# Optimization experiments

Measured on AMD Instinct MI355X. Metric: run time of the kernel, lower is better.

The kernel has to match this reference:

```python
import jax, jax.numpy as jnp
import numpy as np

B, E, H, NH, HD = 8, 1536, 256, 8, 32
L, V, NL, FF = 50, 50257, 4, 2048
BOS = 50256
EPS = 1e-5


def setup_inputs():
    key = jax.random.key(0)
    ks = jax.random.split(key, 12)
    s = 0.02

    def rn(k, shape):
        return jax.random.normal(k, shape, jnp.float32) * s

    return {
        "embedding": jax.random.normal(ks[0], (B, E), jnp.float32),
        "w_proj": rn(ks[1], (H, E)), "b_proj": jnp.zeros((H,), jnp.float32),
        "tok_emb": rn(ks[2], (V, H)),
        "pos_enc": rn(ks[3], (1, L, H)),
        "sa_in_w": rn(ks[4], (NL, 3 * H, H)), "sa_in_b": jnp.zeros((NL, 3 * H), jnp.float32),
        "sa_out_w": rn(ks[5], (NL, H, H)), "sa_out_b": jnp.zeros((NL, H), jnp.float32),
        "ca_in_w": rn(ks[6], (NL, 3 * H, H)), "ca_in_b": jnp.zeros((NL, 3 * H), jnp.float32),
        "ca_out_w": rn(ks[7], (NL, H, H)), "ca_out_b": jnp.zeros((NL, H), jnp.float32),
        "ff1_w": rn(ks[8], (NL, FF, H)), "ff1_b": jnp.zeros((NL, FF), jnp.float32),
        "ff2_w": rn(ks[9], (NL, H, FF)), "ff2_b": jnp.zeros((NL, H), jnp.float32),
        "ln_g": jnp.ones((NL, 3, H), jnp.float32), "ln_b": jnp.zeros((NL, 3, H), jnp.float32),
        "fc_w": rn(ks[10], (V, H)), "fc_b": jnp.zeros((V,), jnp.float32),
    }


def _ln(x, g, b):
    m = jnp.mean(x, -1, keepdims=True)
    v = jnp.mean((x - m) ** 2, -1, keepdims=True)
    return (x - m) * jax.lax.rsqrt(v + EPS) * g + b


def _mha(q_in, kv_in, in_w, in_b, out_w, out_b, mask):
    wq, wk, wv = jnp.split(in_w, 3, axis=0)
    bq, bk, bv = jnp.split(in_b, 3)

    def heads(t):
        b_, l_, _ = t.shape
        return t.reshape(b_, l_, NH, HD).transpose(0, 2, 1, 3)  # [B,NH,L,HD]

    q = heads(q_in @ wq.T + bq)
    k = heads(kv_in @ wk.T + bk)
    v = heads(kv_in @ wv.T + bv)
    scores = jnp.einsum('bhqd,bhkd->bhqk', q, k) * (1.0 / np.sqrt(HD))
    if mask is not None:
        scores = scores + mask
    a = jax.nn.softmax(scores, axis=-1)
    o = jnp.einsum('bhqk,bhkd->bhqd', a, v)
    o = o.transpose(0, 2, 1, 3).reshape(q_in.shape)
    return o @ out_w.T + out_b


def _decoder(x, mem, mask, p):
    # nn.TransformerDecoderLayer, post-LN, relu FFN
    for l in range(NL):
        x = _ln(x + _mha(x, x, p['sa_in_w'][l], p['sa_in_b'][l], p['sa_out_w'][l], p['sa_out_b'][l], mask), p['ln_g'][l, 0], p['ln_b'][l, 0])
        x = _ln(x + _mha(x, mem, p['ca_in_w'][l], p['ca_in_b'][l], p['ca_out_w'][l], p['ca_out_b'][l], None), p['ln_g'][l, 1], p['ln_b'][l, 1])
        h = jax.nn.relu(x @ p['ff1_w'][l].T + p['ff1_b'][l]) @ p['ff2_w'][l].T + p['ff2_b'][l]
        x = _ln(x + h, p['ln_g'][l, 2], p['ln_b'][l, 2])
    return x


def _forward(embedding, tok_emb, pos_enc, w_proj, b_proj, fc_w, fc_b, p):
    mem = (embedding @ w_proj.T + b_proj)[:, None, :]  # [B,1,H] single-token memory
    causal = jnp.tril(jnp.ones((L, L), bool))
    mask = jnp.where(causal, 0.0, -jnp.inf)[None, None]  # [1,1,L,L]
    tokens0 = jnp.full((B, L), BOS, jnp.int32)  # padded token buffer; pos 0 = BOS

    # At step t the original recomputes the decoder over the first t+1 tokens and
    # reads the last position. With a causal mask, position t of a full-length
    # decode depends only on tokens[:t+1], so decoding the padded buffer and
    # slicing position t is exactly the same math (no-KV-cache recompute kept).
    def step(tokens, t):
        x = tok_emb[tokens] + pos_enc[:, :L]
        x = _decoder(x, mem, mask, p)
        h_t = jax.lax.dynamic_slice_in_dim(x, t, 1, axis=1)[:, 0]  # [B,H]
        logits = h_t @ fc_w.T + fc_b  # [B,V]
        nxt = jnp.argmax(logits, -1).astype(jnp.int32)
        tokens = jax.lax.dynamic_update_slice_in_dim(tokens, nxt[:, None], t + 1, axis=1)
        return tokens, logits

    _, logits = jax.lax.scan(step, tokens0, jnp.arange(L - 1))
    return jnp.transpose(logits, (1, 0, 2))  # [B, L-1, V]


def reference(embedding, w_proj, b_proj, tok_emb, pos_enc, sa_in_w, sa_in_b, sa_out_w, sa_out_b, ca_in_w, ca_in_b, ca_out_w, ca_out_b, ff1_w, ff1_b, ff2_w, ff2_b, ln_g, ln_b, fc_w, fc_b):
    p = dict(sa_in_w=sa_in_w, sa_in_b=sa_in_b, sa_out_w=sa_out_w, sa_out_b=sa_out_b,
             ca_in_w=ca_in_w, ca_in_b=ca_in_b, ca_out_w=ca_out_w, ca_out_b=ca_out_b,
             ff1_w=ff1_w, ff1_b=ff1_b, ff2_w=ff2_w, ff2_b=ff2_b, ln_g=ln_g, ln_b=ln_b)
    return _forward(embedding, tok_emb, pos_enc, w_proj, b_proj, fc_w, fc_b, p)
```

## Files before the change

### kernel.cpp

```cpp
#include <hip/hip_runtime.h>

#define NV 50257
#define BOSTOK 50256
#define LNEPS 1e-5f
#define NSTEP 49
#define NBLK 256
#define RPB 197
#define DYN_LDS_BYTES ((256 * 52 + 50 * 256) * 4)
#define FSTR 64

#define FQKV(l)   (0 + (l))
#define FU(l)     (4 + (l))
#define FFPX(l,j) (8 + (l) * 8 + (j))
#define FXF(j)    (40 + (j))
#define FFC(j)    (48 + (j))
#define FMEMF     56
#define FCAF      57

#define WS4_MEM 4096
#define WS4_CA  6144
#define WS4_XF  14336
#define WS4_Q   16384
#define WS4_K   18432
#define WS4_V   20480
#define WS4_U   22528
#define WS4_FFP 30720
#define WS4_PV  63488
#define WS4_PI  65536

__device__ __forceinline__ float gld(const float* p) {
  return __hip_atomic_load(const_cast<float*>(p), __ATOMIC_RELAXED, __HIP_MEMORY_SCOPE_AGENT);
}
__device__ __forceinline__ void gst(float* p, float v) {
  __hip_atomic_store(p, v, __ATOMIC_RELAXED, __HIP_MEMORY_SCOPE_AGENT);
}
__device__ __forceinline__ void gsti(int* p, int v) {
  __hip_atomic_store(p, v, __ATOMIC_RELAXED, __HIP_MEMORY_SCOPE_AGENT);
}
__device__ __forceinline__ unsigned fld(unsigned* p) {
  return __hip_atomic_load(p, __ATOMIC_RELAXED, __HIP_MEMORY_SCOPE_AGENT);
}
__device__ __forceinline__ void bump(unsigned* f) {
  asm volatile("s_waitcnt vmcnt(0)" ::: "memory");
  __syncthreads();
  if (threadIdx.x == 0)
    __hip_atomic_fetch_add(f, 1u, __ATOMIC_RELAXED, __HIP_MEMORY_SCOPE_AGENT);
}
__device__ __forceinline__ void bump8(unsigned* f) {
  asm volatile("s_waitcnt vmcnt(0)" ::: "memory");
  __syncthreads();
  if (threadIdx.x == 0)
    for (int j = 0; j < 8; ++j)
      __hip_atomic_fetch_add(f + j * FSTR, 1u, __ATOMIC_RELAXED, __HIP_MEMORY_SCOPE_AGENT);
}
__device__ __forceinline__ unsigned waitf(unsigned* f, unsigned tgt, unsigned* sh) {
  if (threadIdx.x == 0) {
    unsigned v = fld(f);
    while (v < tgt) { __builtin_amdgcn_s_sleep(1); v = fld(f); }
    *sh = v;
  }
  __syncthreads();
  return *sh;
}
__device__ __forceinline__ unsigned wait_fcsum(unsigned* FL, unsigned tgt, unsigned* sh) {
  if (threadIdx.x == 0) {
    unsigned s;
    for (;;) {
      s = 0;
      for (int j = 0; j < 8; ++j) s += fld(FL + (48 + j) * FSTR);
      if (s >= tgt) break;
      __builtin_amdgcn_s_sleep(1);
    }
    *sh = s;
  }
  __syncthreads();
  return *sh;
}

__device__ __forceinline__ void pull2p(float* x, float* y,
    const float* p0, const float* p1, unsigned salt) {
  asm("global_load_dword %0, %2, off sc0 sc1\n\t"
      "global_load_dword %1, %3, off sc0 sc1\n\t"
      "s_waitcnt vmcnt(0)"
      : "=&v"(*x), "=&v"(*y)
      : "v"(p0), "v"(p1), "v"(salt));
}
__device__ __forceinline__ void pull3p(float* x, float* y, float* z,
    const float* p0, const float* p1, const float* p2, unsigned salt) {
  asm("global_load_dword %0, %3, off sc0 sc1\n\t"
      "global_load_dword %1, %4, off sc0 sc1\n\t"
      "global_load_dword %2, %5, off sc0 sc1\n\t"
      "s_waitcnt vmcnt(0)"
      : "=&v"(*x), "=&v"(*y), "=&v"(*z)
      : "v"(p0), "v"(p1), "v"(p2), "v"(salt));
}
__device__ __forceinline__ void pull8p(float r[8],
    const float* p0, const float* p1, const float* p2, const float* p3,
    const float* p4, const float* p5, const float* p6, const float* p7, unsigned salt) {
  float a0, a1, a2, a3, a4, a5, a6, a7;
  asm("global_load_dword %0, %8, off sc0 sc1\n\t"
      "global_load_dword %1, %9, off sc0 sc1\n\t"
      "global_load_dword %2, %10, off sc0 sc1\n\t"
      "global_load_dword %3, %11, off sc0 sc1\n\t"
      "global_load_dword %4, %12, off sc0 sc1\n\t"
      "global_load_dword %5, %13, off sc0 sc1\n\t"
      "global_load_dword %6, %14, off sc0 sc1\n\t"
      "global_load_dword %7, %15, off sc0 sc1\n\t"
      "s_waitcnt vmcnt(0)"
      : "=&v"(a0), "=&v"(a1), "=&v"(a2), "=&v"(a3),
        "=&v"(a4), "=&v"(a5), "=&v"(a6), "=&v"(a7)
      : "v"(p0), "v"(p1), "v"(p2), "v"(p3), "v"(p4), "v"(p5), "v"(p6), "v"(p7), "v"(salt));
  r[0] = a0; r[1] = a1; r[2] = a2; r[3] = a3;
  r[4] = a4; r[5] = a5; r[6] = a6; r[7] = a7;
}
__device__ __forceinline__ void pull1_2q(float* u, float4* f0, float4* f1,
    const float* pu, const float* pf, unsigned salt) {
  asm("global_load_dword %0, %3, off sc0 sc1\n\t"
      "global_load_dwordx4 %1, %4, off sc0 sc1\n\t"
      "global_load_dwordx4 %2, %4, off offset:16 sc0 sc1\n\t"
      "s_waitcnt vmcnt(0)"
      : "=&v"(*u), "=&v"(*f0), "=&v"(*f1)
      : "v"(pu), "v"(pf), "v"(salt));
}
__device__ __forceinline__ void pull4x8(float4 r[8],
    const float* p0, const float* p1, const float* p2, const float* p3, unsigned salt) {
  float4 a0, a1, a2, a3, a4, a5, a6, a7;
  asm("global_load_dwordx4 %0, %8, off sc0 sc1\n\t"
      "global_load_dwordx4 %1, %8, off offset:16 sc0 sc1\n\t"
      "global_load_dwordx4 %2, %9, off sc0 sc1\n\t"
      "global_load_dwordx4 %3, %9, off offset:16 sc0 sc1\n\t"
      "global_load_dwordx4 %4, %10, off sc0 sc1\n\t"
      "global_load_dwordx4 %5, %10, off offset:16 sc0 sc1\n\t"
      "global_load_dwordx4 %6, %11, off sc0 sc1\n\t"
      "global_load_dwordx4 %7, %11, off offset:16 sc0 sc1\n\t"
      "s_waitcnt vmcnt(0)"
      : "=&v"(a0), "=&v"(a1), "=&v"(a2), "=&v"(a3),
        "=&v"(a4), "=&v"(a5), "=&v"(a6), "=&v"(a7)
      : "v"(p0), "v"(p1), "v"(p2), "v"(p3), "v"(salt));
  r[0] = a0; r[1] = a1; r[2] = a2; r[3] = a3;
  r[4] = a4; r[5] = a5; r[6] = a6; r[7] = a7;
}

__device__ __forceinline__ float block_ln256(float v, int tid, float* red8, float g, float bta) {
  float s = v, s2 = v * v;
#pragma unroll
  for (int m = 32; m >= 1; m >>= 1) { s += __shfl_xor(s, m); s2 += __shfl_xor(s2, m); }
  int w = tid >> 6;
  __syncthreads();
  if ((tid & 63) == 0) { red8[w] = s; red8[4 + w] = s2; }
  __syncthreads();
  s = red8[0] + red8[1] + red8[2] + red8[3];
  s2 = red8[4] + red8[5] + red8[6] + red8[7];
  float mn = s * (1.0f / 256.0f);
  float var = s2 * (1.0f / 256.0f) - mn * mn;
  float rs = rsqrtf(var + LNEPS);
  return (v - mn) * rs * g + bta;
}

__device__ __forceinline__ void fc_phase(int bid, int tid, int t, unsigned salt,
                                         const float* xf, const float* fc_w,
                                         const float* fc_b, float* out,
                                         float* pv, int* pi,
                                         float* xl, float* rv, int* ri) {
  {
    float xv8[8];
    pull8p(xv8, xf + 0 * 256 + tid, xf + 1 * 256 + tid, xf + 2 * 256 + tid, xf + 3 * 256 + tid,
           xf + 4 * 256 + tid, xf + 5 * 256 + tid, xf + 6 * 256 + tid, xf + 7 * 256 + tid, salt);
#pragma unroll
    for (int b = 0; b < 8; ++b) xl[b * 260 + tid] = xv8[b];
  }
  __syncthreads();
  int r = tid >> 3, b = tid & 7;
  float bv = -3e38f; int bi = 2147483647;
  int base = bid * RPB;
  for (int i = 0; i < 7; ++i) {
    int rr = i * 32 + r, row = base + rr;
    if (rr < RPB && row < NV) {
      float acc = fc_b[row];
      const float4* w4 = reinterpret_cast<const float4*>(fc_w + (size_t)row * 256);
      const float4* xv = reinterpret_cast<const float4*>(xl + b * 260);
      for (int k = 0; k < 64; ++k) {
        float4 wv = w4[k]; float4 xq = xv[k];
        acc += wv.x * xq.x + wv.y * xq.y + wv.z * xq.z + wv.w * xq.w;
      }
      out[(size_t)(b * 49 + t) * NV + row] = acc;
      if (acc > bv || (acc == bv && row < bi)) { bv = acc; bi = row; }
    }
  }
  rv[tid] = bv; ri[tid] = bi;
  __syncthreads();
  for (int off = 128; off >= 8; off >>= 1) {
    if (tid < off) {
      float v = rv[tid + off]; int id = ri[tid + off];
      if (v > rv[tid] || (v == rv[tid] && id < ri[tid])) { rv[tid] = v; ri[tid] = id; }
    }
    __syncthreads();
  }
  if (tid < 8) { gst(pv + bid * 8 + tid, rv[tid]); gsti(pi + bid * 8 + tid, ri[tid]); }
}

__global__ __launch_bounds__(256) void k_flow4(
    const float* __restrict__ emb, const float* __restrict__ w_proj, const float* __restrict__ b_proj,
    const float* __restrict__ tok_emb, const float* __restrict__ pos_enc,
    const float* __restrict__ sa_in_w, const float* __restrict__ sa_in_b,
    const float* __restrict__ sa_out_w, const float* __restrict__ sa_out_b,
    const float* __restrict__ ca_in_w, const float* __restrict__ ca_in_b,
    const float* __restrict__ ca_out_w, const float* __restrict__ ca_out_b,
    const float* __restrict__ ff1_w, const float* __restrict__ ff1_b,
    const float* __restrict__ ff2_w, const float* __restrict__ ff2_b,
    const float* __restrict__ ln_g, const float* __restrict__ ln_b,
    const float* __restrict__ fc_w, const float* __restrict__ fc_b,
    float* __restrict__ out, float* __restrict__ wsf, int* __restrict__ wsi) {
  extern __shared__ float dynlds[];
  const int bid = blockIdx.x, tid = threadIdx.x;

  unsigned* FL = (unsigned*)wsf;
  float* mem = wsf + WS4_MEM;
  float* ca  = wsf + WS4_CA;
  float* xf  = wsf + WS4_XF;
  float* qb  = wsf + WS4_Q;
  float* kb  = wsf + WS4_K;
  float* vb  = wsf + WS4_V;
  float* u   = wsf + WS4_U;
  float* ffp = wsf + WS4_FFP;
  float* pv  = wsf + WS4_PV;
  int*   pi  = wsi + WS4_PI;

  __shared__ float xl[8 * 260];
  __shared__ float h1l[256 * 9];
  __shared__ float ql[256], ol[256], ph[8 * 64];
  __shared__ float red8[8];
  __shared__ float rv[256];
  __shared__ int   ri[256];
  __shared__ int   toks[8];
  __shared__ unsigned saltsh;
  __shared__ float el[1536];

  if (bid < 64) {
    int b = bid >> 3, tile = bid & 7;
    for (int k = tid; k < 1536; k += 256) el[k] = emb[b * 1536 + k];
    __syncthreads();
    int r = tid >> 3, g = tid & 7;
    int row = tile * 32 + r;
    float acc = 0.f;
    const float* wr = w_proj + (size_t)row * 1536;
    for (int c = g * 192; c < g * 192 + 192; ++c) acc += wr[c] * el[c];
    rv[tid] = acc;
    __syncthreads();
    for (int off = 4; off >= 1; off >>= 1) {
      if (g < off) rv[tid] += rv[tid + off];
      __syncthreads();
    }
    if (g == 0) gst(mem + b * 256 + row, rv[tid] + b_proj[row]);
    bump(FL + FMEMF * FSTR);
  }
  if (bid >= 64 && bid < 96) {
    unsigned s0 = waitf(FL + FMEMF * FSTR, 64u, &saltsh);
    int l = (bid - 64) >> 3, b = (bid - 64) & 7;
    ql[tid] = gld(mem + b * 256 + tid) + 0.f * (float)(s0 & 0);
    __syncthreads();
    float acc = ca_in_b[l * 768 + 512 + tid];
    const float* wr = ca_in_w + (size_t)(l * 768 + 512 + tid) * 256;
    for (int c = 0; c < 256; ++c) acc += wr[c] * ql[c];
    ol[tid] = acc;
    __syncthreads();
    float acc2 = ca_out_b[l * 256 + tid];
    const float* wr2 = ca_out_w + (size_t)(l * 256 + tid) * 256;
    for (int c = 0; c < 256; ++c) acc2 += wr2[c] * ol[c];
    gst(ca + (l * 8 + b) * 256 + tid, acc2);
    bump(FL + FCAF * FSTR);
  }

  if (bid < 32) {
    int myl = bid >> 3, myb = bid & 7;
    float* Klds = dynlds;
    float* Vlds = dynlds + 256 * 52;
    unsigned sc = waitf(FL + FCAF * FSTR, 32u, &saltsh);
    float caval = gld(ca + ((myl * 8 + myb) * 256 + (int)(sc & 0)) + tid);
    for (int t = 0; t < NSTEP; ++t) {
      float xres;
      if (myl == 0) {
        if (t > 0) {
          unsigned s = wait_fcsum(FL, 256u * (unsigned)t, &saltsh);
          float pvv, piv;
          pull2p(&pvv, &piv, pv + tid * 8 + myb, (const float*)(pi + tid * 8 + myb), s);
          rv[tid] = pvv; ri[tid] = __float_as_int(piv);
          __syncthreads();
          for (int off = 128; off >= 1; off >>= 1) {
            if (tid < off) {
              float v = rv[tid + off]; int id = ri[tid + off];
              if (v > rv[tid] || (v == rv[tid] && id < ri[tid])) { rv[tid] = v; ri[tid] = id; }
            }
            __syncthreads();
          }
          if (tid == 0) toks[0] = ri[0];
          __syncthreads();
        } else {
          if (tid == 0) toks[0] = BOSTOK;
          __syncthreads();
        }
        xres = tok_emb[(size_t)toks[0] * 256 + tid] + pos_enc[t * 256 + tid];
      } else {
        unsigned s = waitf(FL + FFPX(myl - 1, bid & 7) * FSTR, 8u * (unsigned)(t + 1), &saltsh);
        float uv; float4 f0, f1;
        int par = (myl - 1) & 1;
        pull1_2q(&uv, &f0, &f1, u + (myl - 1) * 2048 + myb * 256 + tid,
                 ffp + par * 16384 + (myb * 256 + tid) * 8, s);
        float a = uv + ff2_b[(myl - 1) * 256 + tid]
                + f0.x + f0.y + f0.z + f0.w + f1.x + f1.y + f1.z + f1.w;
        xres = block_ln256(a, tid, red8, ln_g[((myl - 1) * 3 + 2) * 256 + tid],
                           ln_b[((myl - 1) * 3 + 2) * 256 + tid]);
      }
      unsigned s2 = waitf(FL + FQKV(myl) * FSTR, 24u * (unsigned)(t + 1), &saltsh);
      float qv, kv, vv;
      pull3p(&qv, &kv, &vv, qb + myb * 256 + tid, kb + myb * 256 + tid, vb + myb * 256 + tid, s2);
      ql[tid] = qv;
      Klds[tid * 52 + t] = kv;
      Vlds[t * 256 + tid] = vv;
      __syncthreads();
      int h = tid >> 5, j0 = tid & 31;
      const float* qh = ql + h * 32;
      float s0v = -3e38f, s1v = -3e38f;
      if (j0 <= t) {
        float d0 = 0.f;
#pragma unroll
        for (int d = 0; d < 32; ++d) d0 += qh[d] * Klds[(h * 32 + d) * 52 + j0];
        s0v = d0 * 0.17677669529663687f;
      }
      if (j0 + 32 <= t) {
        float d1 = 0.f;
#pragma unroll
        for (int d = 0; d < 32; ++d) d1 += qh[d] * Klds[(h * 32 + d) * 52 + j0 + 32];
        s1v = d1 * 0.17677669529663687f;
      }
      float mx = fmaxf(s0v, s1v);
      for (int m = 16; m >= 1; m >>= 1) mx = fmaxf(mx, __shfl_xor(mx, m, 32));
      float e0 = (j0 <= t) ? expf(s0v - mx) : 0.f;
      float e1 = (j0 + 32 <= t) ? expf(s1v - mx) : 0.f;
      float sm = e0 + e1;
      for (int m = 16; m >= 1; m >>= 1) sm += __shfl_xor(sm, m, 32);
      ph[h * 64 + j0] = e0;
      ph[h * 64 + j0 + 32] = e1;
      __syncthreads();
      float o = 0.f;
      for (int j = 0; j <= t; ++j) o += ph[h * 64 + j] * Vlds[j * 256 + tid];
      ol[tid] = o / sm;
      __syncthreads();
      float acc = sa_out_b[myl * 256 + tid];
      const float4* w4 = reinterpret_cast<const float4*>(sa_out_w + (size_t)(myl * 256 + tid) * 256);
#pragma unroll 4
      for (int k = 0; k < 64; ++k) {
        float4 wv = w4[k];
        acc += wv.x * ol[4 * k] + wv.y * ol[4 * k + 1] + wv.z * ol[4 * k + 2] + wv.w * ol[4 * k + 3];
      }
      acc += xres;
      float y = block_ln256(acc, tid, red8, ln_g[(myl * 3 + 0) * 256 + tid],
                            ln_b[(myl * 3 + 0) * 256 + tid]);
      float y2 = block_ln256(y + caval, tid, red8,
                             ln_g[(myl * 3 + 1) * 256 + tid], ln_b[(myl * 3 + 1) * 256 + tid]);
      gst(u + myl * 2048 + myb * 256 + tid, y2);
      bump(FL + FU(myl) * FSTR);

      if (myl == 0) {
        unsigned s3 = waitf(FL + FFPX(3, bid & 7) * FSTR, 8u * (unsigned)(t + 1), &saltsh);
        float uv; float4 f0, f1;
        pull1_2q(&uv, &f0, &f1, u + 3 * 2048 + myb * 256 + tid,
                 ffp + 1 * 16384 + (myb * 256 + tid) * 8, s3);
        float a = uv + ff2_b[3 * 256 + tid]
                + f0.x + f0.y + f0.z + f0.w + f1.x + f1.y + f1.z + f1.w;
        float xfv = block_ln256(a, tid, red8, ln_g[(3 * 3 + 2) * 256 + tid],
                                ln_b[(3 * 3 + 2) * 256 + tid]);
        gst(xf + myb * 256 + tid, xfv);
        bump8(FL + FXF(0) * FSTR);
      }
      unsigned s4 = waitf(FL + FXF(bid & 7) * FSTR, 8u * (unsigned)(t + 1), &saltsh);
      fc_phase(bid, tid, t, s4, xf, fc_w, fc_b, out, pv, pi, xl, rv, ri);
      bump(FL + FFC(bid & 7) * FSTR);
    }
  } else if (bid < 56) {
    int qi = bid - 32;
    for (int t = 0; t < NSTEP; ++t) {
      for (int l = 0; l < 4; ++l) {
        if (l == 0) {
          if (t == 0) {
            if (tid < 8) toks[tid] = BOSTOK;
            __syncthreads();
          } else {
            unsigned s = wait_fcsum(FL, 256u * (unsigned)t, &saltsh);
            int i0 = tid >> 3, b = tid & 7;
            float pvv[8], piv[8];
            pull8p(pvv, pv + (i0 + 0) * 8 + b, pv + (i0 + 32) * 8 + b, pv + (i0 + 64) * 8 + b,
                   pv + (i0 + 96) * 8 + b, pv + (i0 + 128) * 8 + b, pv + (i0 + 160) * 8 + b,
                   pv + (i0 + 192) * 8 + b, pv + (i0 + 224) * 8 + b, s);
            const float* pif = (const float*)pi;
            pull8p(piv, pif + (i0 + 0) * 8 + b, pif + (i0 + 32) * 8 + b, pif + (i0 + 64) * 8 + b,
                   pif + (i0 + 96) * 8 + b, pif + (i0 + 128) * 8 + b, pif + (i0 + 160) * 8 + b,
                   pif + (i0 + 192) * 8 + b, pif + (i0 + 224) * 8 + b, s);
            float bv = -3e38f; int bi = 2147483647;
#pragma unroll
            for (int k = 0; k < 8; ++k) {
              float v = pvv[k]; int id = __float_as_int(piv[k]);
              if (v > bv || (v == bv && id < bi)) { bv = v; bi = id; }
            }
            rv[tid] = bv; ri[tid] = bi;
            __syncthreads();
            for (int off = 128; off >= 8; off >>= 1) {
              if (tid < off) {
                float v = rv[tid + off]; int id = ri[tid + off];
                if (v > rv[tid] || (v == rv[tid] && id < ri[tid])) { rv[tid] = v; ri[tid] = id; }
              }
              __syncthreads();
            }
            if (tid < 8) toks[tid] = ri[tid];
            __syncthreads();
          }
          for (int b = 0; b < 8; ++b)
            xl[b * 260 + tid] = tok_emb[(size_t)toks[b] * 256 + tid] + pos_enc[t * 256 + tid];
          __syncthreads();
        } else {
          unsigned s = waitf(FL + FFPX(l - 1, bid & 7) * FSTR, 8u * (unsigned)(t + 1), &saltsh);
          int lp = l - 1, par = lp & 1;
          float u8[8];
          pull8p(u8, u + lp * 2048 + 0 * 256 + tid, u + lp * 2048 + 1 * 256 + tid,
                 u + lp * 2048 + 2 * 256 + tid, u + lp * 2048 + 3 * 256 + tid,
                 u + lp * 2048 + 4 * 256 + tid, u + lp * 2048 + 5 * 256 + tid,
                 u + lp * 2048 + 6 * 256 + tid, u + lp * 2048 + 7 * 256 + tid, s);
          float4 fA[8], fB[8];
          const float* fb = ffp + par * 16384;
          pull4x8(fA, fb + (0 * 256 + tid) * 8, fb + (1 * 256 + tid) * 8,
                  fb + (2 * 256 + tid) * 8, fb + (3 * 256 + tid) * 8, s);
          pull4x8(fB, fb + (4 * 256 + tid) * 8, fb + (5 * 256 + tid) * 8,
                  fb + (6 * 256 + tid) * 8, fb + (7 * 256 + tid) * 8, s);
          float g = ln_g[(lp * 3 + 2) * 256 + tid], bt = ln_b[(lp * 3 + 2) * 256 + tid];
          float f2b = ff2_b[lp * 256 + tid];
#pragma unroll
          for (int b = 0; b < 8; ++b) {
            float4 q0 = (b < 4) ? fA[2 * b] : fB[2 * (b - 4)];
            float4 q1 = (b < 4) ? fA[2 * b + 1] : fB[2 * (b - 4) + 1];
            float a = u8[b] + f2b + q0.x + q0.y + q0.z + q0.w + q1.x + q1.y + q1.z + q1.w;
            xl[b * 260 + tid] = block_ln256(a, tid, red8, g, bt);
          }
          __syncthreads();
        }
        int r = tid >> 3, b8 = tid & 7;
        int row = qi * 32 + r;
        float acc = sa_in_b[l * 768 + row];
        const float4* w4 = reinterpret_cast<const float4*>(sa_in_w + (size_t)(l * 768 + row) * 256);
        const float4* xv = reinterpret_cast<const float4*>(xl + b8 * 260);
#pragma unroll 8
        for (int k = 0; k < 64; ++k) {
          float4 wv = w4[k]; float4 xq = xv[k];
          acc += wv.x * xq.x + wv.y * xq.y + wv.z * xq.z + wv.w * xq.w;
        }
        if (row < 256) gst(qb + b8 * 256 + row, acc);
        else if (row < 512) gst(kb + b8 * 256 + (row - 256), acc);
        else gst(vb + b8 * 256 + (row - 512), acc);
        bump(FL + FQKV(l) * FSTR);
      }
      unsigned s4 = waitf(FL + FXF(bid & 7) * FSTR, 8u * (unsigned)(t + 1), &saltsh);
      fc_phase(bid, tid, t, s4, xf, fc_w, fc_b, out, pv, pi, xl, rv, ri);
      bump(FL + FFC(bid & 7) * FSTR);
    }
  } else if (bid < 64) {
    int s = bid - 56;
    for (int t = 0; t < NSTEP; ++t) {
      for (int l = 0; l < 4; ++l) {
        unsigned sv = waitf(FL + FU(l) * FSTR, 8u * (unsigned)(t + 1), &saltsh);
        {
          float u8[8];
          pull8p(u8, u + l * 2048 + 0 * 256 + tid, u + l * 2048 + 1 * 256 + tid,
                 u + l * 2048 + 2 * 256 + tid, u + l * 2048 + 3 * 256 + tid,
                 u + l * 2048 + 4 * 256 + tid, u + l * 2048 + 5 * 256 + tid,
                 u + l * 2048 + 6 * 256 + tid, u + l * 2048 + 7 * 256 + tid, sv);
#pragma unroll
          for (int b = 0; b < 8; ++b) xl[b * 260 + tid] = u8[b];
        }
        __syncthreads();
        {
          int row = s * 256 + tid;
          float acc[8];
          float bb = ff1_b[l * 2048 + row];
#pragma unroll
          for (int b = 0; b < 8; ++b) acc[b] = bb;
          const float4* w4 = reinterpret_cast<const float4*>(ff1_w + (size_t)(l * 2048 + row) * 256);
          for (int k = 0; k < 64; ++k) {
            float4 wv = w4[k];
#pragma unroll
            for (int b = 0; b < 8; ++b) {
              const float4 xq = reinterpret_cast<const float4*>(xl + b * 260)[k];
              acc[b] += wv.x * xq.x + wv.y * xq.y + wv.z * xq.z + wv.w * xq.w;
            }
          }
#pragma unroll
          for (int b = 0; b < 8; ++b) h1l[tid * 9 + b] = fmaxf(acc[b], 0.f);
        }
        __syncthreads();
        {
          float facc[8] = {0, 0, 0, 0, 0, 0, 0, 0};
          const float* w2p = ff2_w + (size_t)(l * 256 + tid) * 2048 + s * 256;
          for (int n = 0; n < 256; ++n) {
            float wv = w2p[n];
#pragma unroll
            for (int b = 0; b < 8; ++b) facc[b] += wv * h1l[n * 9 + b];
          }
          int par = l & 1;
#pragma unroll
          for (int b = 0; b < 8; ++b)
            gst(ffp + par * 16384 + (b * 256 + tid) * 8 + s, facc[b]);
        }
        bump8(FL + FFPX(l, 0) * FSTR);
        __syncthreads();
      }
      unsigned s4 = waitf(FL + FXF(bid & 7) * FSTR, 8u * (unsigned)(t + 1), &saltsh);
      fc_phase(bid, tid, t, s4, xf, fc_w, fc_b, out, pv, pi, xl, rv, ri);
      bump(FL + FFC(bid & 7) * FSTR);
    }
  } else {
    for (int t = 0; t < NSTEP; ++t) {
      unsigned s4 = waitf(FL + FXF(bid & 7) * FSTR, 8u * (unsigned)(t + 1), &saltsh);
      fc_phase(bid, tid, t, s4, xf, fc_w, fc_b, out, pv, pi, xl, rv, ri);
      bump(FL + FFC(bid & 7) * FSTR);
    }
  }
}

extern "C" void kernel_launch(void* const* d_in, const int* in_sizes, int n_in,
                              void* d_out, int out_size, void* d_ws, size_t ws_size,
                              hipStream_t stream) {
  (void)in_sizes; (void)n_in; (void)out_size; (void)ws_size;
  const float* embedding = (const float*)d_in[0];
  const float* w_proj   = (const float*)d_in[1];
  const float* b_proj   = (const float*)d_in[2];
  const float* tok_emb  = (const float*)d_in[3];
  const float* pos_enc  = (const float*)d_in[4];
  const float* sa_in_w  = (const float*)d_in[5];
  const float* sa_in_b  = (const float*)d_in[6];
  const float* sa_out_w = (const float*)d_in[7];
  const float* sa_out_b = (const float*)d_in[8];
  const float* ca_in_w  = (const float*)d_in[9];
  const float* ca_in_b  = (const float*)d_in[10];
  const float* ca_out_w = (const float*)d_in[11];
  const float* ca_out_b = (const float*)d_in[12];
  const float* ff1_w    = (const float*)d_in[13];
  const float* ff1_b    = (const float*)d_in[14];
  const float* ff2_w    = (const float*)d_in[15];
  const float* ff2_b    = (const float*)d_in[16];
  const float* ln_g     = (const float*)d_in[17];
  const float* ln_b     = (const float*)d_in[18];
  const float* fc_w     = (const float*)d_in[19];
  const float* fc_b     = (const float*)d_in[20];
  float* out = (float*)d_out;
  float* wsf = (float*)d_ws;
  int*   wsi = (int*)d_ws;

  (void)hipFuncSetAttribute(reinterpret_cast<const void*>(k_flow4),
                            hipFuncAttributeMaxDynamicSharedMemorySize, DYN_LDS_BYTES);
  (void)hipMemsetAsync(d_ws, 0, 16384, stream);
  hipLaunchKernelGGL(k_flow4, dim3(NBLK), dim3(256), DYN_LDS_BYTES, stream,
                     embedding, w_proj, b_proj, tok_emb, pos_enc,
                     sa_in_w, sa_in_b, sa_out_w, sa_out_b,
                     ca_in_w, ca_in_b, ca_out_w, ca_out_b,
                     ff1_w, ff1_b, ff2_w, ff2_b,
                     ln_g, ln_b, fc_w, fc_b,
                     out, wsf, wsi);
}
```

Baseline: 10.72 ms.

## Fuse final LayerNorm into every FC block and replace sleep-based polling with spinning

Each of the 256 blocks now computes the final-layer residual and LayerNorm for all 8 batch rows itself, right before its vocab-projection slice. Previously 32 blocks computed it, published it to a global buffer and raised a separate flag. Removing that extra flag handoff takes one cross-block synchronisation hop off the critical path of every decode step. In exchange every block repeats the LN work and reads more global data. Separately, flag polling now busy-spins on FMA bursts instead of s_sleep, and the eight FC counter flags are read with a single batched asm load sequence, both aimed at cutting wake-up latency at the cost of more power and memory traffic from spinning.

```diff
diff --git a/kernel.cpp b/kernel.cpp
--- a/kernel.cpp
+++ b/kernel.cpp
@@ -12,7 +12,6 @@
 #define FQKV(l)   (0 + (l))
 #define FU(l)     (4 + (l))
 #define FFPX(l,j) (8 + (l) * 8 + (j))
-#define FXF(j)    (40 + (j))
 #define FFC(j)    (48 + (j))
 #define FMEMF     56
 #define FCAF      57
@@ -40,6 +39,11 @@
 __device__ __forceinline__ unsigned fld(unsigned* p) {
   return __hip_atomic_load(p, __ATOMIC_RELAXED, __HIP_MEMORY_SCOPE_AGENT);
 }
+__device__ __forceinline__ void spin_burst(float z) {
+#pragma unroll
+  for (int i = 0; i < 64; ++i) z = __builtin_fmaf(z, 1.0000001f, 1e-30f);
+  asm volatile("" :: "v"(z));
+}
 __device__ __forceinline__ void bump(unsigned* f) {
   asm volatile("s_waitcnt vmcnt(0)" ::: "memory");
   __syncthreads();
@@ -56,7 +60,7 @@
 __device__ __forceinline__ unsigned waitf(unsigned* f, unsigned tgt, unsigned* sh) {
   if (threadIdx.x == 0) {
     unsigned v = fld(f);
-    while (v < tgt) { __builtin_amdgcn_s_sleep(1); v = fld(f); }
+    while (v < tgt) { spin_burst((float)v); v = fld(f); }
     *sh = v;
   }
   __syncthreads();
@@ -64,12 +68,26 @@
 }
 __device__ __forceinline__ unsigned wait_fcsum(unsigned* FL, unsigned tgt, unsigned* sh) {
   if (threadIdx.x == 0) {
+    const unsigned* bp = FL + 48 * FSTR;
     unsigned s;
     for (;;) {
-      s = 0;
-      for (int j = 0; j < 8; ++j) s += fld(FL + (48 + j) * FSTR);
+      unsigned a0, a1, a2, a3, a4, a5, a6, a7;
+      asm volatile(
+          "global_load_dword %0, %8, off sc0 sc1\n\t"
+          "global_load_dword %1, %8, off offset:256 sc0 sc1\n\t"
+          "global_load_dword %2, %8, off offset:512 sc0 sc1\n\t"
+          "global_load_dword %3, %8, off offset:768 sc0 sc1\n\t"
+          "global_load_dword %4, %8, off offset:1024 sc0 sc1\n\t"
+          "global_load_dword %5, %8, off offset:1280 sc0 sc1\n\t"
+          "global_load_dword %6, %8, off offset:1536 sc0 sc1\n\t"
+          "global_load_dword %7, %8, off offset:1792 sc0 sc1\n\t"
+          "s_waitcnt vmcnt(0)"
+          : "=&v"(a0), "=&v"(a1), "=&v"(a2), "=&v"(a3),
+            "=&v"(a4), "=&v"(a5), "=&v"(a6), "=&v"(a7)
+          : "v"(bp) : "memory");
+      s = a0 + a1 + a2 + a3 + a4 + a5 + a6 + a7;
       if (s >= tgt) break;
-      __builtin_amdgcn_s_sleep(1);
+      spin_burst((float)s);
     }
     *sh = s;
   }
@@ -157,17 +175,34 @@
   return (v - mn) * rs * g + bta;
 }
 
-__device__ __forceinline__ void fc_phase(int bid, int tid, int t, unsigned salt,
-                                         const float* xf, const float* fc_w,
-                                         const float* fc_b, float* out,
-                                         float* pv, int* pi,
-                                         float* xl, float* rv, int* ri) {
+__device__ __forceinline__ void finalln_fc(int bid, int tid, int t, unsigned salt,
+                                           const float* u, const float* ffp,
+                                           const float* ff2_b, const float* ln_g,
+                                           const float* ln_b,
+                                           const float* fc_w, const float* fc_b, float* out,
+                                           float* pv, int* pi,
+                                           float* xl, float* rv, int* ri, float* red8) {
   {
-    float xv8[8];
-    pull8p(xv8, xf + 0 * 256 + tid, xf + 1 * 256 + tid, xf + 2 * 256 + tid, xf + 3 * 256 + tid,
-           xf + 4 * 256 + tid, xf + 5 * 256 + tid, xf + 6 * 256 + tid, xf + 7 * 256 + tid, salt);
-#pragma unroll
-    for (int b = 0; b < 8; ++b) xl[b * 260 + tid] = xv8[b];
+    float u8[8];
+    pull8p(u8, u + 3 * 2048 + 0 * 256 + tid, u + 3 * 2048 + 1 * 256 + tid,
+           u + 3 * 2048 + 2 * 256 + tid, u + 3 * 2048 + 3 * 256 + tid,
+           u + 3 * 2048 + 4 * 256 + tid, u + 3 * 2048 + 5 * 256 + tid,
+           u + 3 * 2048 + 6 * 256 + tid, u + 3 * 2048 + 7 * 256 + tid, salt);
+    float4 fA[8], fB[8];
+    const float* fb = ffp + 1 * 16384;
+    pull4x8(fA, fb + (0 * 256 + tid) * 8, fb + (1 * 256 + tid) * 8,
+            fb + (2 * 256 + tid) * 8, fb + (3 * 256 + tid) * 8, salt);
+    pull4x8(fB, fb + (4 * 256 + tid) * 8, fb + (5 * 256 + tid) * 8,
+            fb + (6 * 256 + tid) * 8, fb + (7 * 256 + tid) * 8, salt);
+    float g = ln_g[(3 * 3 + 2) * 256 + tid], bt = ln_b[(3 * 3 + 2) * 256 + tid];
+    float f2b = ff2_b[3 * 256 + tid];
+#pragma unroll
+    for (int b = 0; b < 8; ++b) {
+      float4 q0 = (b < 4) ? fA[2 * b] : fB[2 * (b - 4)];
+      float4 q1 = (b < 4) ? fA[2 * b + 1] : fB[2 * (b - 4) + 1];
+      float a = u8[b] + f2b + q0.x + q0.y + q0.z + q0.w + q1.x + q1.y + q1.z + q1.w;
+      xl[b * 260 + tid] = block_ln256(a, tid, red8, g, bt);
+    }
   }
   __syncthreads();
   int r = tid >> 3, b = tid & 7;
@@ -199,7 +234,7 @@
   if (tid < 8) { gst(pv + bid * 8 + tid, rv[tid]); gsti(pi + bid * 8 + tid, ri[tid]); }
 }
 
-__global__ __launch_bounds__(256) void k_flow4(
+__global__ __launch_bounds__(256) void k_flow6(
     const float* __restrict__ emb, const float* __restrict__ w_proj, const float* __restrict__ b_proj,
     const float* __restrict__ tok_emb, const float* __restrict__ pos_enc,
     const float* __restrict__ sa_in_w, const float* __restrict__ sa_in_b,
@@ -217,7 +252,6 @@
   unsigned* FL = (unsigned*)wsf;
   float* mem = wsf + WS4_MEM;
   float* ca  = wsf + WS4_CA;
-  float* xf  = wsf + WS4_XF;
   float* qb  = wsf + WS4_Q;
   float* kb  = wsf + WS4_K;
   float* vb  = wsf + WS4_V;
@@ -361,20 +395,9 @@
       gst(u + myl * 2048 + myb * 256 + tid, y2);
       bump(FL + FU(myl) * FSTR);
 
-      if (myl == 0) {
-        unsigned s3 = waitf(FL + FFPX(3, bid & 7) * FSTR, 8u * (unsigned)(t + 1), &saltsh);
-        float uv; float4 f0, f1;
-        pull1_2q(&uv, &f0, &f1, u + 3 * 2048 + myb * 256 + tid,
-                 ffp + 1 * 16384 + (myb * 256 + tid) * 8, s3);
-        float a = uv + ff2_b[3 * 256 + tid]
-                + f0.x + f0.y + f0.z + f0.w + f1.x + f1.y + f1.z + f1.w;
-        float xfv = block_ln256(a, tid, red8, ln_g[(3 * 3 + 2) * 256 + tid],
-                                ln_b[(3 * 3 + 2) * 256 + tid]);
-        gst(xf + myb * 256 + tid, xfv);
-        bump8(FL + FXF(0) * FSTR);
-      }
-      unsigned s4 = waitf(FL + FXF(bid & 7) * FSTR, 8u * (unsigned)(t + 1), &saltsh);
-      fc_phase(bid, tid, t, s4, xf, fc_w, fc_b, out, pv, pi, xl, rv, ri);
+      unsigned s4 = waitf(FL + FFPX(3, bid & 7) * FSTR, 8u * (unsigned)(t + 1), &saltsh);
+      finalln_fc(bid, tid, t, s4, u, ffp, ff2_b, ln_g, ln_b, fc_w, fc_b, out, pv, pi,
+                 xl, rv, ri, red8);
       bump(FL + FFC(bid & 7) * FSTR);
     }
   } else if (bid < 56) {
@@ -457,8 +480,9 @@
         else gst(vb + b8 * 256 + (row - 512), acc);
         bump(FL + FQKV(l) * FSTR);
       }
-      unsigned s4 = waitf(FL + FXF(bid & 7) * FSTR, 8u * (unsigned)(t + 1), &saltsh);
-      fc_phase(bid, tid, t, s4, xf, fc_w, fc_b, out, pv, pi, xl, rv, ri);
+      unsigned s4 = waitf(FL + FFPX(3, bid & 7) * FSTR, 8u * (unsigned)(t + 1), &saltsh);
+      finalln_fc(bid, tid, t, s4, u, ffp, ff2_b, ln_g, ln_b, fc_w, fc_b, out, pv, pi,
+                 xl, rv, ri, red8);
       bump(FL + FFC(bid & 7) * FSTR);
     }
   } else if (bid < 64) {
@@ -511,14 +535,16 @@
         bump8(FL + FFPX(l, 0) * FSTR);
         __syncthreads();
       }
-      unsigned s4 = waitf(FL + FXF(bid & 7) * FSTR, 8u * (unsigned)(t + 1), &saltsh);
-      fc_phase(bid, tid, t, s4, xf, fc_w, fc_b, out, pv, pi, xl, rv, ri);
+      unsigned s4 = waitf(FL + FFPX(3, bid & 7) * FSTR, 8u * (unsigned)(t + 1), &saltsh);
+      finalln_fc(bid, tid, t, s4, u, ffp, ff2_b, ln_g, ln_b, fc_w, fc_b, out, pv, pi,
+                 xl, rv, ri, red8);
       bump(FL + FFC(bid & 7) * FSTR);
     }
   } else {
     for (int t = 0; t < NSTEP; ++t) {
-      unsigned s4 = waitf(FL + FXF(bid & 7) * FSTR, 8u * (unsigned)(t + 1), &saltsh);
-      fc_phase(bid, tid, t, s4, xf, fc_w, fc_b, out, pv, pi, xl, rv, ri);
+      unsigned s4 = waitf(FL + FFPX(3, bid & 7) * FSTR, 8u * (unsigned)(t + 1), &saltsh);
+      finalln_fc(bid, tid, t, s4, u, ffp, ff2_b, ln_g, ln_b, fc_w, fc_b, out, pv, pi,
+                 xl, rv, ri, red8);
       bump(FL + FFC(bid & 7) * FSTR);
     }
   }
@@ -553,10 +579,10 @@
   float* wsf = (float*)d_ws;
   int*   wsi = (int*)d_ws;
 
-  (void)hipFuncSetAttribute(reinterpret_cast<const void*>(k_flow4),
+  (void)hipFuncSetAttribute(reinterpret_cast<const void*>(k_flow6),
                             hipFuncAttributeMaxDynamicSharedMemorySize, DYN_LDS_BYTES);
   (void)hipMemsetAsync(d_ws, 0, 16384, stream);
-  hipLaunchKernelGGL(k_flow4, dim3(NBLK), dim3(256), DYN_LDS_BYTES, stream,
+  hipLaunchKernelGGL(k_flow6, dim3(NBLK), dim3(256), DYN_LDS_BYTES, stream,
                      embedding, w_proj, b_proj, tok_emb, pos_enc,
                      sa_in_w, sa_in_b, sa_out_w, sa_out_b,
                      ca_in_w, ca_in_b, ca_out_w, ca_out_b,
```

After: 10.75 ms. Within noise of the previous version (+0.3%).
